# Kernel optimization log

Hardware: AMD Instinct MI355X
Metric: run time of the kernel (lower is better)

Reference implementation:

```python
import jax, jax.numpy as jnp
import numpy as np

EPS = 1e-8

def squash(s, axis=-1):
    sq = jnp.sum(s * s, axis=axis, keepdims=True)
    return sq / (1.0 + sq) * s / (jnp.sqrt(sq) + EPS)

def setup_inputs() -> dict:
    key = jax.random.key(0)
    k1, k2 = jax.random.split(key)
    B, in_caps, in_dim = 256, 1152, 8
    num_caps, dim_caps = 10, 16
    x = jax.random.normal(k1, (B, in_caps, in_dim), dtype=jnp.float32)
    W = 0.01 * jax.random.normal(k2, (num_caps, in_caps, dim_caps, in_dim), dtype=jnp.float32)
    return {"x": x, "W": W}

def reference(x, W, num_routing=3):
    # u_hat: [B, num_caps, in_caps, dim_caps]
    u_hat = jnp.einsum('ncdi,bci->bncd', W, x)
    u_hat_det = jax.lax.stop_gradient(u_hat)
    B, N, C, D = u_hat.shape
    b = jnp.zeros((B, N, C, 1), dtype=u_hat.dtype)
    for _ in range(num_routing - 1):
        c = jax.nn.softmax(b, axis=1)                 # over num_caps
        s = jnp.sum(c * u_hat_det, axis=2)            # [B, N, D]
        v = squash(s)
        uv = jnp.einsum('bncd,bnd->bnc', u_hat_det, v)[..., None]
        b = b + uv
    c = jax.nn.softmax(b, axis=1)
    s = jnp.sum(c * u_hat, axis=2)
    v = squash(s)                                     # [B, N, D]
    return v
```

## Files before the change

### kernel.cpp

```cpp
#include <hip/hip_runtime.h>
#include <math.h>
#include <stdint.h>

#define B_N 256
#define C_N 1152
#define I_N 8
#define N_N 10
#define D_N 16

constexpr int C_CHUNKS = 48;
constexpr int C_PER    = 24;
constexpr int STAGE_C  = 12;
constexpr int N_STAGES = 2;
constexpr int B_TILE   = 16;
constexpr int BLOCK    = 256;

typedef short v8s __attribute__((ext_vector_type(8)));
typedef float v4f __attribute__((ext_vector_type(4)));

constexpr int POOL_BYTES = 30720 + 6400 + 7824;

__device__ __forceinline__ uint32_t bf16_rne(float f) {
    uint32_t u = __float_as_uint(f);
    return (u + 0x7FFFu + ((u >> 16) & 1u)) >> 16;
}
__device__ __forceinline__ uint32_t pack2(float a, float b) {
    return bf16_rne(a) | (bf16_rne(b) << 16);
}
__device__ __forceinline__ float bf2f(short s) {
    return __uint_as_float(((uint32_t)(uint16_t)s) << 16);
}

template <bool FIRST>
__global__ __launch_bounds__(BLOCK, 3)
void route_pass(const float* __restrict__ x, const float* __restrict__ W,
                const float* __restrict__ vsum, float* __restrict__ p_s)
{
    __shared__ __align__(16) char pool[POOL_BYTES];
    short* Ws   = (short*)pool;
    short* xs   = (short*)(pool + 30720);
    float* cfl  = (float*)(pool + 37120);
    float* comb = (float*)(pool + 30720);

    const int tid   = threadIdx.x;
    const int wv    = tid >> 6;
    const int lane  = tid & 63;
    const int b     = lane & 15;
    const int quad  = lane >> 4;
    const int chunk = blockIdx.x;
    const int gb0   = blockIdx.y * B_TILE;
    const int c0    = chunk * C_PER;

    {
        const float4* x4 = reinterpret_cast<const float4*>(x);
        #pragma unroll
        for (int it = 0; it < 3; ++it) {
            int e = (tid + BLOCK * it) * 4;
            int b2 = e / 192, r = e - b2 * 192;
            float4 v = x4[((size_t)(gb0 + b2) * (C_N * I_N) + c0 * I_N + r) >> 2];
            *reinterpret_cast<uint2*>(xs + b2 * 200 + r) =
                make_uint2(pack2(v.x, v.y), pack2(v.z, v.w));
        }
    }

    v4f vs[N_N];
    if (!FIRST) {
        #pragma unroll
        for (int n = 0; n < N_N; ++n) {
            const float4 t = *reinterpret_cast<const float4*>(
                vsum + (((size_t)(gb0 + b) * N_N + n) * D_N + quad * 4));
            vs[n] = (v4f){t.x, t.y, t.z, t.w};
        }
    }

    const int ncnt = (wv < 2) ? 3 : 2;
    v4f sacc[3];
    sacc[0] = (v4f){0.f, 0.f, 0.f, 0.f};
    sacc[1] = (v4f){0.f, 0.f, 0.f, 0.f};
    sacc[2] = (v4f){0.f, 0.f, 0.f, 0.f};

    const float4* W4 = reinterpret_cast<const float4*>(W);

    for (int st = 0; st < N_STAGES; ++st) {
        __syncthreads();
        #pragma unroll
        for (int it = 0; it < 15; ++it) {
            int e = (tid + BLOCK * it) * 4;
            int n = e / 1536, rr = e - n * 1536;
            int c = rr >> 7, k = rr & 127;
            float4 v = W4[((size_t)n * (C_N * 128) + (size_t)(c0 + st * STAGE_C + c) * 128 + k) >> 2];
            *reinterpret_cast<uint2*>(Ws + c * 1280 + n * 128 + k) =
                make_uint2(pack2(v.x, v.y), pack2(v.z, v.w));
        }
        __syncthreads();

        if (!FIRST) {
            #pragma unroll
            for (int t = 0; t < 3; ++t) {
                const int cl = wv + 4 * t;
                const v8s xb = *reinterpret_cast<const v8s*>(
                    xs + b * 200 + (st * STAGE_C + cl) * 8);
                float Z = 0.f;
                #pragma unroll
                for (int n = 0; n < N_N; ++n) {
                    v8s wa = {0, 0, 0, 0, 0, 0, 0, 0};
                    if (quad == 0)
                        wa = *reinterpret_cast<const v8s*>(Ws + cl * 1280 + n * 128 + b * 8);
                    v4f u = __builtin_amdgcn_mfma_f32_16x16x32_bf16(
                        wa, xb, (v4f){0.f, 0.f, 0.f, 0.f}, 0, 0, 0);
                    float l = u[0] * vs[n][0] + u[1] * vs[n][1]
                            + u[2] * vs[n][2] + u[3] * vs[n][3];
                    l += __shfl_xor(l, 16);
                    l += __shfl_xor(l, 32);
                    const float e1 = __expf(l);
                    Z += e1;
                    if ((n & 3) == quad)
                        cfl[cl * 163 + n * 16 + b] = e1;
                }
                const float rz = __builtin_amdgcn_rcpf(Z);
                #pragma unroll
                for (int jj = 0; jj < 3; ++jj) {
                    int n = 4 * jj + quad;
                    if (n < N_N) cfl[cl * 163 + n * 16 + b] *= rz;
                }
            }
        }
        __syncthreads();

        #pragma unroll
        for (int Q = 0; Q < 3; ++Q) {
            const int clq   = Q * 4 + quad;
            const int cfull = st * STAGE_C + clq;
            const v8s xq = *reinterpret_cast<const v8s*>(xs + b * 200 + cfull * 8);
            float xf[8];
            #pragma unroll
            for (int j = 0; j < 8; ++j) xf[j] = bf2f(xq[j]);
            #pragma unroll
            for (int jj = 0; jj < 3; ++jj) {
                if (jj < ncnt) {
                    const int n = wv + 4 * jj;
                    const float cv = FIRST ? 0.1f : cfl[clq * 163 + n * 16 + b];
                    union { v8s s; uint32_t u[4]; } zu;
                    zu.u[0] = pack2(cv * xf[0], cv * xf[1]);
                    zu.u[1] = pack2(cv * xf[2], cv * xf[3]);
                    zu.u[2] = pack2(cv * xf[4], cv * xf[5]);
                    zu.u[3] = pack2(cv * xf[6], cv * xf[7]);
                    const v8s wa = *reinterpret_cast<const v8s*>(
                        Ws + clq * 1280 + n * 128 + b * 8);
                    sacc[jj] = __builtin_amdgcn_mfma_f32_16x16x32_bf16(
                        wa, zu.s, sacc[jj], 0, 0, 0);
                }
            }
        }
    }

    __syncthreads();
    #pragma unroll
    for (int jj = 0; jj < 3; ++jj) {
        if (jj < ncnt) {
            const int n = wv + 4 * jj;
            #pragma unroll
            for (int r = 0; r < 4; ++r)
                comb[b * 163 + n * 16 + quad * 4 + r] = sacc[jj][r];
        }
    }
    __syncthreads();
    #pragma unroll
    for (int k = 0; k < 10; ++k) {
        int e = tid + BLOCK * k;
        int bb = e / 160, rem = e - bb * 160;
        p_s[((size_t)chunk * B_N + gb0 + bb) * 160 + rem] = comb[bb * 163 + rem];
    }
}

__global__ __launch_bounds__(BLOCK)
void reduce_squash(const float* __restrict__ p_s, float* __restrict__ vsum,
                   float* __restrict__ out, int phase)
{
    const int warp = threadIdx.x >> 6;
    const int lane = threadIdx.x & 63;
    const int g    = blockIdx.x * 4 + warp;
    const int q    = lane & 3;
    const int h    = lane >> 2;

    float4 s = make_float4(0.f, 0.f, 0.f, 0.f);
    #pragma unroll
    for (int m = 0; m < C_CHUNKS / 16; ++m) {
        const int cc = h + 16 * m;
        float4 v = *reinterpret_cast<const float4*>(
            &p_s[((size_t)cc * (B_N * N_N) + g) * D_N + q * 4]);
        s.x += v.x; s.y += v.y; s.z += v.z; s.w += v.w;
    }
    #pragma unroll
    for (int off = 4; off < 64; off <<= 1) {
        s.x += __shfl_xor(s.x, off);
        s.y += __shfl_xor(s.y, off);
        s.z += __shfl_xor(s.z, off);
        s.w += __shfl_xor(s.w, off);
    }
    float sq = s.x * s.x + s.y * s.y + s.z * s.z + s.w * s.w;
    sq += __shfl_xor(sq, 1);
    sq += __shfl_xor(sq, 2);

    const float scale = (sq / (1.f + sq)) / (sqrtf(sq) + 1e-8f);
    const float4 v = make_float4(scale * s.x, scale * s.y, scale * s.z, scale * s.w);

    if (h == 0) {
        if (phase == 0) {
            *reinterpret_cast<float4*>(&vsum[(size_t)g * D_N + q * 4]) = v;
        } else if (phase == 1) {
            float4 o = *reinterpret_cast<const float4*>(&vsum[(size_t)g * D_N + q * 4]);
            *reinterpret_cast<float4*>(&vsum[(size_t)g * D_N + q * 4]) =
                make_float4(o.x + v.x, o.y + v.y, o.z + v.z, o.w + v.w);
        } else {
            *reinterpret_cast<float4*>(&out[(size_t)g * D_N + q * 4]) = v;
        }
    }
}

extern "C" void kernel_launch(void* const* d_in, const int* in_sizes, int n_in,
                              void* d_out, int out_size, void* d_ws, size_t ws_size,
                              hipStream_t stream)
{
    const float* x = (const float*)d_in[0];
    const float* W = (const float*)d_in[1];
    float* out  = (float*)d_out;
    float* vsum = (float*)d_ws;
    float* p_s  = vsum + (size_t)B_N * N_N * D_N;

    dim3 grid(C_CHUNKS, B_N / B_TILE);
    dim3 blk(BLOCK);
    dim3 rgrid((B_N * N_N) / 4);

    route_pass<true><<<grid, blk, 0, stream>>>(x, W, nullptr, p_s);
    reduce_squash<<<rgrid, blk, 0, stream>>>(p_s, vsum, out, 0);
    route_pass<false><<<grid, blk, 0, stream>>>(x, W, vsum, p_s);
    reduce_squash<<<rgrid, blk, 0, stream>>>(p_s, vsum, out, 1);
    route_pass<false><<<grid, blk, 0, stream>>>(x, W, vsum, p_s);
    reduce_squash<<<rgrid, blk, 0, stream>>>(p_s, vsum, out, 2);
}
```

Before: 134.8 us.

## Retile routing pass to 12 capsules by 32 batches to reuse W more

Each block now stages W for 12 input capsules once and reuses it across 32 batch rows processed as two 16-row halves, instead of 24 capsules in two stages across 16 rows. This halves global W traffic and removes the per-stage LDS reload and its barriers. LDS strides are padded (1288, 33, 164) to reduce bank conflicts. In exchange, the number of capsule chunks doubles, so partial-sum writes to p_s and the reduce_squash reads also double, and per-thread accumulator registers increase.

```diff
diff --git a/kernel.cpp b/kernel.cpp
--- a/kernel.cpp
+++ b/kernel.cpp
@@ -8,17 +8,15 @@
 #define N_N 10
 #define D_N 16
 
-constexpr int C_CHUNKS = 48;
-constexpr int C_PER    = 24;
-constexpr int STAGE_C  = 12;
-constexpr int N_STAGES = 2;
-constexpr int B_TILE   = 16;
+constexpr int C_PER    = 12;
+constexpr int C_CHUNKS = C_N / C_PER;
+constexpr int B_TILE   = 32;
 constexpr int BLOCK    = 256;
 
 typedef short v8s __attribute__((ext_vector_type(8)));
 typedef float v4f __attribute__((ext_vector_type(4)));
 
-constexpr int POOL_BYTES = 30720 + 6400 + 7824;
+constexpr int POOL_BYTES = 30912 + 6400 + 15840;
 
 __device__ __forceinline__ uint32_t bf16_rne(float f) {
     uint32_t u = __float_as_uint(f);
@@ -38,9 +36,9 @@
 {
     __shared__ __align__(16) char pool[POOL_BYTES];
     short* Ws   = (short*)pool;
-    short* xs   = (short*)(pool + 30720);
-    float* cfl  = (float*)(pool + 37120);
-    float* comb = (float*)(pool + 30720);
+    short* xs   = (short*)(pool + 30912);
+    float* cfl  = (float*)(pool + 37312);
+    float* comb = (float*)(pool + 30912);
 
     const int tid   = threadIdx.x;
     const int wv    = tid >> 6;
@@ -56,56 +54,49 @@
         #pragma unroll
         for (int it = 0; it < 3; ++it) {
             int e = (tid + BLOCK * it) * 4;
-            int b2 = e / 192, r = e - b2 * 192;
-            float4 v = x4[((size_t)(gb0 + b2) * (C_N * I_N) + c0 * I_N + r) >> 2];
-            *reinterpret_cast<uint2*>(xs + b2 * 200 + r) =
+            int b2 = e / 96, r = e - b2 * 96;
+            float4 v = x4[(size_t)(gb0 + b2) * 2304 + chunk * 24 + (r >> 2)];
+            *reinterpret_cast<uint2*>(xs + b2 * 100 + r) =
                 make_uint2(pack2(v.x, v.y), pack2(v.z, v.w));
         }
     }
-
-    v4f vs[N_N];
-    if (!FIRST) {
-        #pragma unroll
-        for (int n = 0; n < N_N; ++n) {
-            const float4 t = *reinterpret_cast<const float4*>(
-                vsum + (((size_t)(gb0 + b) * N_N + n) * D_N + quad * 4));
-            vs[n] = (v4f){t.x, t.y, t.z, t.w};
-        }
-    }
-
-    const int ncnt = (wv < 2) ? 3 : 2;
-    v4f sacc[3];
-    sacc[0] = (v4f){0.f, 0.f, 0.f, 0.f};
-    sacc[1] = (v4f){0.f, 0.f, 0.f, 0.f};
-    sacc[2] = (v4f){0.f, 0.f, 0.f, 0.f};
-
-    const float4* W4 = reinterpret_cast<const float4*>(W);
-
-    for (int st = 0; st < N_STAGES; ++st) {
-        __syncthreads();
+    {
+        const float4* W4 = reinterpret_cast<const float4*>(W);
         #pragma unroll
         for (int it = 0; it < 15; ++it) {
             int e = (tid + BLOCK * it) * 4;
             int n = e / 1536, rr = e - n * 1536;
             int c = rr >> 7, k = rr & 127;
-            float4 v = W4[((size_t)n * (C_N * 128) + (size_t)(c0 + st * STAGE_C + c) * 128 + k) >> 2];
-            *reinterpret_cast<uint2*>(Ws + c * 1280 + n * 128 + k) =
+            float4 v = W4[(size_t)n * 36864 + (size_t)(c0 + c) * 32 + (k >> 2)];
+            *reinterpret_cast<uint2*>(Ws + c * 1288 + n * 128 + k) =
                 make_uint2(pack2(v.x, v.y), pack2(v.z, v.w));
         }
-        __syncthreads();
-
-        if (!FIRST) {
+    }
+    __syncthreads();
+
+    const int ncnt = (wv < 2) ? 3 : 2;
+
+    if (!FIRST) {
+        #pragma unroll
+        for (int T = 0; T < 2; ++T) {
+            v4f vs[N_N];
+            #pragma unroll
+            for (int n = 0; n < N_N; ++n) {
+                const float4 t4 = *reinterpret_cast<const float4*>(
+                    vsum + (((size_t)(gb0 + T * 16 + b) * N_N + n) * D_N + quad * 4));
+                vs[n] = (v4f){t4.x, t4.y, t4.z, t4.w};
+            }
             #pragma unroll
             for (int t = 0; t < 3; ++t) {
                 const int cl = wv + 4 * t;
                 const v8s xb = *reinterpret_cast<const v8s*>(
-                    xs + b * 200 + (st * STAGE_C + cl) * 8);
+                    xs + (T * 16 + b) * 100 + cl * 8);
                 float Z = 0.f;
                 #pragma unroll
                 for (int n = 0; n < N_N; ++n) {
                     v8s wa = {0, 0, 0, 0, 0, 0, 0, 0};
                     if (quad == 0)
-                        wa = *reinterpret_cast<const v8s*>(Ws + cl * 1280 + n * 128 + b * 8);
+                        wa = *reinterpret_cast<const v8s*>(Ws + cl * 1288 + n * 128 + b * 8);
                     v4f u = __builtin_amdgcn_mfma_f32_16x16x32_bf16(
                         wa, xb, (v4f){0.f, 0.f, 0.f, 0.f}, 0, 0, 0);
                     float l = u[0] * vs[n][0] + u[1] * vs[n][1]
@@ -115,23 +106,32 @@
                     const float e1 = __expf(l);
                     Z += e1;
                     if ((n & 3) == quad)
-                        cfl[cl * 163 + n * 16 + b] = e1;
+                        cfl[cl * 330 + n * 33 + T * 16 + b] = e1;
                 }
                 const float rz = __builtin_amdgcn_rcpf(Z);
                 #pragma unroll
                 for (int jj = 0; jj < 3; ++jj) {
                     int n = 4 * jj + quad;
-                    if (n < N_N) cfl[cl * 163 + n * 16 + b] *= rz;
+                    if (n < N_N) cfl[cl * 330 + n * 33 + T * 16 + b] *= rz;
                 }
             }
         }
         __syncthreads();
-
+    }
+
+    v4f sacc[2][3];
+    #pragma unroll
+    for (int T = 0; T < 2; ++T)
+        #pragma unroll
+        for (int jj = 0; jj < 3; ++jj) sacc[T][jj] = (v4f){0.f, 0.f, 0.f, 0.f};
+
+    #pragma unroll
+    for (int T = 0; T < 2; ++T) {
         #pragma unroll
         for (int Q = 0; Q < 3; ++Q) {
-            const int clq   = Q * 4 + quad;
-            const int cfull = st * STAGE_C + clq;
-            const v8s xq = *reinterpret_cast<const v8s*>(xs + b * 200 + cfull * 8);
+            const int clq = Q * 4 + quad;
+            const v8s xq = *reinterpret_cast<const v8s*>(
+                xs + (T * 16 + b) * 100 + clq * 8);
             float xf[8];
             #pragma unroll
             for (int j = 0; j < 8; ++j) xf[j] = bf2f(xq[j]);
@@ -139,16 +139,17 @@
             for (int jj = 0; jj < 3; ++jj) {
                 if (jj < ncnt) {
                     const int n = wv + 4 * jj;
-                    const float cv = FIRST ? 0.1f : cfl[clq * 163 + n * 16 + b];
+                    const float cv = FIRST ? 0.1f
+                        : cfl[clq * 330 + n * 33 + T * 16 + b];
                     union { v8s s; uint32_t u[4]; } zu;
                     zu.u[0] = pack2(cv * xf[0], cv * xf[1]);
                     zu.u[1] = pack2(cv * xf[2], cv * xf[3]);
                     zu.u[2] = pack2(cv * xf[4], cv * xf[5]);
                     zu.u[3] = pack2(cv * xf[6], cv * xf[7]);
                     const v8s wa = *reinterpret_cast<const v8s*>(
-                        Ws + clq * 1280 + n * 128 + b * 8);
-                    sacc[jj] = __builtin_amdgcn_mfma_f32_16x16x32_bf16(
-                        wa, zu.s, sacc[jj], 0, 0, 0);
+                        Ws + clq * 1288 + n * 128 + b * 8);
+                    sacc[T][jj] = __builtin_amdgcn_mfma_f32_16x16x32_bf16(
+                        wa, zu.s, sacc[T][jj], 0, 0, 0);
                 }
             }
         }
@@ -156,20 +157,22 @@
 
     __syncthreads();
     #pragma unroll
-    for (int jj = 0; jj < 3; ++jj) {
-        if (jj < ncnt) {
-            const int n = wv + 4 * jj;
-            #pragma unroll
-            for (int r = 0; r < 4; ++r)
-                comb[b * 163 + n * 16 + quad * 4 + r] = sacc[jj][r];
-        }
-    }
+    for (int T = 0; T < 2; ++T)
+        #pragma unroll
+        for (int jj = 0; jj < 3; ++jj) {
+            if (jj < ncnt) {
+                const int n = wv + 4 * jj;
+                #pragma unroll
+                for (int r = 0; r < 4; ++r)
+                    comb[(T * 16 + b) * 164 + n * 16 + quad * 4 + r] = sacc[T][jj][r];
+            }
+        }
     __syncthreads();
     #pragma unroll
-    for (int k = 0; k < 10; ++k) {
+    for (int k = 0; k < 20; ++k) {
         int e = tid + BLOCK * k;
         int bb = e / 160, rem = e - bb * 160;
-        p_s[((size_t)chunk * B_N + gb0 + bb) * 160 + rem] = comb[bb * 163 + rem];
+        p_s[((size_t)chunk * B_N + gb0 + bb) * 160 + rem] = comb[bb * 164 + rem];
     }
 }
 
```

Result: slower. 139.8 us (+3.7%).

## Halve per-block channel chunk, stage vsum in LDS, vectorize partial stores

Applied to the files above, without the earlier changes.

Cuts the input capsules per block from 24 to 12, processed in three stages of four, which doubles the grid and raises the occupancy target to six blocks per CU through smaller shared memory. The vsum routing vector now goes through shared memory instead of forty registers per thread. Partial-sum writes to the workspace use float4 stores. In exchange, twice as many partial sums are written and then read back by the reduction kernel.

```diff
diff --git a/kernel.cpp b/kernel.cpp
--- a/kernel.cpp
+++ b/kernel.cpp
@@ -8,17 +8,17 @@
 #define N_N 10
 #define D_N 16
 
-constexpr int C_CHUNKS = 48;
-constexpr int C_PER    = 24;
-constexpr int STAGE_C  = 12;
-constexpr int N_STAGES = 2;
+constexpr int C_PER    = 12;
+constexpr int STAGE_C  = 4;
+constexpr int N_STAGES = 3;
+constexpr int C_CHUNKS = C_N / C_PER;
 constexpr int B_TILE   = 16;
 constexpr int BLOCK    = 256;
 
 typedef short v8s __attribute__((ext_vector_type(8)));
 typedef float v4f __attribute__((ext_vector_type(4)));
 
-constexpr int POOL_BYTES = 30720 + 6400 + 7824;
+constexpr int POOL_BYTES = 16176 + 10496;
 
 __device__ __forceinline__ uint32_t bf16_rne(float f) {
     uint32_t u = __float_as_uint(f);
@@ -32,15 +32,16 @@
 }
 
 template <bool FIRST>
-__global__ __launch_bounds__(BLOCK, 3)
+__global__ __launch_bounds__(BLOCK, 6)
 void route_pass(const float* __restrict__ x, const float* __restrict__ W,
                 const float* __restrict__ vsum, float* __restrict__ p_s)
 {
     __shared__ __align__(16) char pool[POOL_BYTES];
     short* Ws   = (short*)pool;
-    short* xs   = (short*)(pool + 30720);
-    float* cfl  = (float*)(pool + 37120);
-    float* comb = (float*)(pool + 30720);
+    short* xs   = (short*)(pool + 10240);
+    float* cfl  = (float*)(pool + 13568);
+    float* vss  = (float*)(pool + 16176);
+    float* comb = (float*)(pool + 0);
 
     const int tid   = threadIdx.x;
     const int wv    = tid >> 6;
@@ -54,22 +55,26 @@
     {
         const float4* x4 = reinterpret_cast<const float4*>(x);
         #pragma unroll
+        for (int it = 0; it < 2; ++it) {
+            int e = (tid + BLOCK * it) * 4;
+            if (e < 1536) {
+                int b2 = e / 96, r = e - b2 * 96;
+                float4 v = x4[(size_t)(gb0 + b2) * 2304 + chunk * 24 + (r >> 2)];
+                *reinterpret_cast<uint2*>(xs + b2 * 104 + r) =
+                    make_uint2(pack2(v.x, v.y), pack2(v.z, v.w));
+            }
+        }
+    }
+    if (!FIRST) {
+        #pragma unroll
         for (int it = 0; it < 3; ++it) {
             int e = (tid + BLOCK * it) * 4;
-            int b2 = e / 192, r = e - b2 * 192;
-            float4 v = x4[((size_t)(gb0 + b2) * (C_N * I_N) + c0 * I_N + r) >> 2];
-            *reinterpret_cast<uint2*>(xs + b2 * 200 + r) =
-                make_uint2(pack2(v.x, v.y), pack2(v.z, v.w));
-        }
-    }
-
-    v4f vs[N_N];
-    if (!FIRST) {
-        #pragma unroll
-        for (int n = 0; n < N_N; ++n) {
-            const float4 t = *reinterpret_cast<const float4*>(
-                vsum + (((size_t)(gb0 + b) * N_N + n) * D_N + quad * 4));
-            vs[n] = (v4f){t.x, t.y, t.z, t.w};
+            if (e < 2560) {
+                int b2 = e / 160, r = e - b2 * 160;
+                float4 v = *reinterpret_cast<const float4*>(
+                    vsum + (size_t)(gb0 + b2) * 160 + r);
+                *reinterpret_cast<float4*>(vss + b2 * 164 + r) = v;
+            }
         }
     }
 
@@ -84,54 +89,50 @@
     for (int st = 0; st < N_STAGES; ++st) {
         __syncthreads();
         #pragma unroll
-        for (int it = 0; it < 15; ++it) {
+        for (int it = 0; it < 5; ++it) {
             int e = (tid + BLOCK * it) * 4;
-            int n = e / 1536, rr = e - n * 1536;
+            int n = e >> 9, rr = e & 511;
             int c = rr >> 7, k = rr & 127;
-            float4 v = W4[((size_t)n * (C_N * 128) + (size_t)(c0 + st * STAGE_C + c) * 128 + k) >> 2];
+            float4 v = W4[(size_t)n * 36864 + (size_t)(c0 + st * STAGE_C + c) * 32 + (k >> 2)];
             *reinterpret_cast<uint2*>(Ws + c * 1280 + n * 128 + k) =
                 make_uint2(pack2(v.x, v.y), pack2(v.z, v.w));
         }
         __syncthreads();
 
         if (!FIRST) {
-            #pragma unroll
-            for (int t = 0; t < 3; ++t) {
-                const int cl = wv + 4 * t;
-                const v8s xb = *reinterpret_cast<const v8s*>(
-                    xs + b * 200 + (st * STAGE_C + cl) * 8);
-                float Z = 0.f;
-                #pragma unroll
-                for (int n = 0; n < N_N; ++n) {
-                    v8s wa = {0, 0, 0, 0, 0, 0, 0, 0};
-                    if (quad == 0)
-                        wa = *reinterpret_cast<const v8s*>(Ws + cl * 1280 + n * 128 + b * 8);
-                    v4f u = __builtin_amdgcn_mfma_f32_16x16x32_bf16(
-                        wa, xb, (v4f){0.f, 0.f, 0.f, 0.f}, 0, 0, 0);
-                    float l = u[0] * vs[n][0] + u[1] * vs[n][1]
-                            + u[2] * vs[n][2] + u[3] * vs[n][3];
-                    l += __shfl_xor(l, 16);
-                    l += __shfl_xor(l, 32);
-                    const float e1 = __expf(l);
-                    Z += e1;
-                    if ((n & 3) == quad)
-                        cfl[cl * 163 + n * 16 + b] = e1;
-                }
-                const float rz = __builtin_amdgcn_rcpf(Z);
-                #pragma unroll
-                for (int jj = 0; jj < 3; ++jj) {
-                    int n = 4 * jj + quad;
-                    if (n < N_N) cfl[cl * 163 + n * 16 + b] *= rz;
-                }
-            }
-        }
-        __syncthreads();
-
-        #pragma unroll
-        for (int Q = 0; Q < 3; ++Q) {
-            const int clq   = Q * 4 + quad;
-            const int cfull = st * STAGE_C + clq;
-            const v8s xq = *reinterpret_cast<const v8s*>(xs + b * 200 + cfull * 8);
+            const int cl = wv;
+            const v8s xb = *reinterpret_cast<const v8s*>(
+                xs + b * 104 + (st * STAGE_C + cl) * 8);
+            float Z = 0.f;
+            #pragma unroll
+            for (int n = 0; n < N_N; ++n) {
+                v8s wa = {0, 0, 0, 0, 0, 0, 0, 0};
+                if (quad == 0)
+                    wa = *reinterpret_cast<const v8s*>(Ws + cl * 1280 + n * 128 + b * 8);
+                v4f u = __builtin_amdgcn_mfma_f32_16x16x32_bf16(
+                    wa, xb, (v4f){0.f, 0.f, 0.f, 0.f}, 0, 0, 0);
+                const float4 vs4 = *reinterpret_cast<const float4*>(
+                    vss + b * 164 + n * 16 + quad * 4);
+                float l = u[0] * vs4.x + u[1] * vs4.y + u[2] * vs4.z + u[3] * vs4.w;
+                l += __shfl_xor(l, 16);
+                l += __shfl_xor(l, 32);
+                const float e1 = __expf(l);
+                Z += e1;
+                if ((n & 3) == quad)
+                    cfl[cl * 163 + n * 16 + b] = e1;
+            }
+            const float rz = __builtin_amdgcn_rcpf(Z);
+            #pragma unroll
+            for (int jj = 0; jj < 3; ++jj) {
+                int n = 4 * jj + quad;
+                if (n < N_N) cfl[cl * 163 + n * 16 + b] *= rz;
+            }
+            __syncthreads();
+        }
+
+        {
+            const int cfull = st * STAGE_C + quad;
+            const v8s xq = *reinterpret_cast<const v8s*>(xs + b * 104 + cfull * 8);
             float xf[8];
             #pragma unroll
             for (int j = 0; j < 8; ++j) xf[j] = bf2f(xq[j]);
@@ -139,14 +140,14 @@
             for (int jj = 0; jj < 3; ++jj) {
                 if (jj < ncnt) {
                     const int n = wv + 4 * jj;
-                    const float cv = FIRST ? 0.1f : cfl[clq * 163 + n * 16 + b];
+                    const float cv = FIRST ? 0.1f : cfl[quad * 163 + n * 16 + b];
                     union { v8s s; uint32_t u[4]; } zu;
                     zu.u[0] = pack2(cv * xf[0], cv * xf[1]);
                     zu.u[1] = pack2(cv * xf[2], cv * xf[3]);
                     zu.u[2] = pack2(cv * xf[4], cv * xf[5]);
                     zu.u[3] = pack2(cv * xf[6], cv * xf[7]);
                     const v8s wa = *reinterpret_cast<const v8s*>(
-                        Ws + clq * 1280 + n * 128 + b * 8);
+                        Ws + quad * 1280 + n * 128 + b * 8);
                     sacc[jj] = __builtin_amdgcn_mfma_f32_16x16x32_bf16(
                         wa, zu.s, sacc[jj], 0, 0, 0);
                 }
@@ -161,15 +162,20 @@
             const int n = wv + 4 * jj;
             #pragma unroll
             for (int r = 0; r < 4; ++r)
-                comb[b * 163 + n * 16 + quad * 4 + r] = sacc[jj][r];
+                comb[b * 164 + n * 16 + quad * 4 + r] = sacc[jj][r];
         }
     }
     __syncthreads();
     #pragma unroll
-    for (int k = 0; k < 10; ++k) {
-        int e = tid + BLOCK * k;
-        int bb = e / 160, rem = e - bb * 160;
-        p_s[((size_t)chunk * B_N + gb0 + bb) * 160 + rem] = comb[bb * 163 + rem];
+    for (int it = 0; it < 3; ++it) {
+        int f = tid + BLOCK * it;
+        if (f < 640) {
+            int e = f * 4;
+            int bb = e / 160, rem = e - bb * 160;
+            float4 v = *reinterpret_cast<const float4*>(comb + bb * 164 + rem);
+            *reinterpret_cast<float4*>(
+                &p_s[((size_t)chunk * B_N + gb0 + bb) * 160 + rem]) = v;
+        }
     }
 }
 
```

Result: no change. 132.6 us (-1.6%).
